# Performance work log

Hardware: AMD Instinct MI355X
Metric: run time of the kernel (lower is better)

The kernel has to match this reference:

```python
import jax, jax.numpy as jnp
import numpy as np

TEMPERATURE = 0.5


def setup_inputs() -> dict:
    key = jax.random.key(0)
    k1, k2 = jax.random.split(key)
    N, D = 8192, 128
    features = jax.random.normal(k1, (N, D), dtype=jnp.float32)
    labels = jax.random.randint(k2, (N,), 0, 10, dtype=jnp.int64)
    return {"features": features, "labels": labels}


def reference(features, labels):
    # cosine similarity via normalized matmul (fused form of the broadcasted version)
    eps = 1e-8
    norm = jnp.maximum(jnp.linalg.norm(features, axis=-1, keepdims=True), eps)
    fn = features / norm
    sim = jnp.einsum('id,jd->ij', fn, fn) / TEMPERATURE  # [N, N]

    pos_mask = labels[:, None] == labels[None, :]        # [N, N] bool
    pos_f = pos_mask.astype(sim.dtype)
    neg_f = 1.0 - pos_f

    exp_pos = jnp.exp(sim * pos_f)                       # [N, N]
    exp_neg = jnp.sum(jnp.exp(sim * neg_f), axis=1, keepdims=True)  # [N, 1]

    loss_mat = -jnp.log(exp_pos / (exp_pos + exp_neg))   # [N, N]
    # mean over positive entries (jit-safe masked mean)
    num_pos = jnp.sum(pos_f)
    loss = jnp.sum(loss_mat * pos_f) / num_pos
    return loss
```

## Files before the change

kernel.cpp:

```cpp
#include <hip/hip_runtime.h>
#include <hip/hip_bf16.h>
#include <math.h>

#define NROWS 8192
#define DIM 128
#define BM 128
#define BN 128
#define CS 8
#define COLS_PER_SLAB (NROWS / CS)
#define CT_ITERS (COLS_PER_SLAB / BN)
#define RS (NROWS / BM)
#define SQRT2 1.41421356237309515f

typedef __attribute__((ext_vector_type(8))) short bf16x8;
typedef __attribute__((ext_vector_type(4))) float f32x4;

__global__ __launch_bounds__(256) void k_norm(const float* __restrict__ f,
                                              __hip_bfloat16* __restrict__ fnb,
                                              float* __restrict__ losssum) {
  if (blockIdx.x == 0 && threadIdx.x == 0) losssum[0] = 0.f;
  int wave = threadIdx.x >> 6;
  int lane = threadIdx.x & 63;
  int row = blockIdx.x * 4 + wave;
  const float* src = f + (size_t)row * DIM;
  float v0 = src[lane];
  float v1 = src[lane + 64];
  float ss = v0 * v0 + v1 * v1;
#pragma unroll
  for (int o = 32; o > 0; o >>= 1) ss += __shfl_down(ss, o);
  ss = __shfl(ss, 0);
  float inv = SQRT2 / fmaxf(sqrtf(ss), 1e-8f);
  __hip_bfloat16* dst = fnb + (size_t)row * DIM;
  dst[lane] = __float2bfloat16(v0 * inv);
  dst[lane + 64] = __float2bfloat16(v1 * inv);
}

__global__ __launch_bounds__(256, 2) void k_main(
    const ushort* __restrict__ fnb, const int* __restrict__ lab,
    float* __restrict__ ptot, float* __restrict__ ppos, float* __restrict__ psim) {
  __shared__ char lds[BM * 256 + BN * 256];
  char* Alds = lds;
  char* Blds = lds + BM * 256;

  const int t = threadIdx.x;
  const int lane = t & 63;
  const int w = t >> 6;
  const int wm = w >> 1;
  const int wn = w & 1;
  const int g = lane >> 4;
  const int li16 = lane & 15;
  const int cs = blockIdx.x;
  const int i0 = blockIdx.y * BM;

  {
    const int4* src = reinterpret_cast<const int4*>(fnb + (size_t)i0 * DIM);
#pragma unroll
    for (int it = 0; it < 8; ++it) {
      int q = t + 256 * it;
      int row = q >> 4, c = q & 15;
      int4 v = src[q];
      *reinterpret_cast<int4*>(Alds + row * 256 + ((c << 4) ^ ((row & 7) << 4))) = v;
    }
  }

  int lr[4][4];
#pragma unroll
  for (int m = 0; m < 4; ++m)
#pragma unroll
    for (int r = 0; r < 4; ++r)
      lr[m][r] = lab[i0 + wm * 64 + m * 16 + g * 4 + r];

  float a_tot[4][4] = {}, a_pos[4][4] = {}, a_sim[4][4] = {};

  for (int ct = 0; ct < CT_ITERS; ++ct) {
    const int j0 = cs * COLS_PER_SLAB + ct * BN;
    __syncthreads();
    {
      const int4* src = reinterpret_cast<const int4*>(fnb + (size_t)j0 * DIM);
#pragma unroll
      for (int it = 0; it < 8; ++it) {
        int q = t + 256 * it;
        int row = q >> 4, c = q & 15;
        int4 v = src[q];
        *reinterpret_cast<int4*>(Blds + row * 256 + ((c << 4) ^ ((row & 7) << 4))) = v;
      }
    }
    __syncthreads();

    f32x4 acc[4][4];
#pragma unroll
    for (int m = 0; m < 4; ++m)
#pragma unroll
      for (int n = 0; n < 4; ++n) acc[m][n] = (f32x4){0.f, 0.f, 0.f, 0.f};

#pragma unroll
    for (int ks = 0; ks < 4; ++ks) {
      const int kb = ks * 64 + (g << 4);
      bf16x8 af[4], bf[4];
#pragma unroll
      for (int m = 0; m < 4; ++m) {
        int r = wm * 64 + m * 16 + li16;
        af[m] = *reinterpret_cast<const bf16x8*>(Alds + r * 256 + (kb ^ ((r & 7) << 4)));
      }
#pragma unroll
      for (int n = 0; n < 4; ++n) {
        int r = wn * 64 + n * 16 + li16;
        bf[n] = *reinterpret_cast<const bf16x8*>(Blds + r * 256 + (kb ^ ((r & 7) << 4)));
      }
#pragma unroll
      for (int m = 0; m < 4; ++m)
#pragma unroll
        for (int n = 0; n < 4; ++n)
          acc[m][n] = __builtin_amdgcn_mfma_f32_16x16x32_bf16(af[m], bf[n], acc[m][n], 0, 0, 0);
    }

#pragma unroll
    for (int n = 0; n < 4; ++n) {
      const int lc = lab[j0 + wn * 64 + n * 16 + li16];
#pragma unroll
      for (int m = 0; m < 4; ++m)
#pragma unroll
        for (int r = 0; r < 4; ++r) {
          float s = acc[m][n][r];
          float E = __expf(s);
          bool pos = (lr[m][r] == lc);
          a_tot[m][r] += E;
          a_pos[m][r] += pos ? E : 0.f;
          a_sim[m][r] += pos ? s : 0.f;
        }
    }
  }

#pragma unroll
  for (int m = 0; m < 4; ++m)
#pragma unroll
    for (int r = 0; r < 4; ++r)
#pragma unroll
      for (int off = 8; off > 0; off >>= 1) {
        a_tot[m][r] += __shfl_xor(a_tot[m][r], off);
        a_pos[m][r] += __shfl_xor(a_pos[m][r], off);
        a_sim[m][r] += __shfl_xor(a_sim[m][r], off);
      }

  __syncthreads();
  float(*red)[2][3] = reinterpret_cast<float(*)[2][3]>(lds);
  if (li16 == 0) {
#pragma unroll
    for (int m = 0; m < 4; ++m)
#pragma unroll
      for (int r = 0; r < 4; ++r) {
        int rl = wm * 64 + m * 16 + g * 4 + r;
        red[rl][wn][0] = a_tot[m][r];
        red[rl][wn][1] = a_pos[m][r];
        red[rl][wn][2] = a_sim[m][r];
      }
  }
  __syncthreads();
  if (wn == 0 && li16 == 0) {
#pragma unroll
    for (int m = 0; m < 4; ++m)
#pragma unroll
      for (int r = 0; r < 4; ++r) {
        int rl = wm * 64 + m * 16 + g * 4 + r;
        int row = i0 + rl;
        ptot[(size_t)cs * NROWS + row] = red[rl][0][0] + red[rl][1][0];
        ppos[(size_t)cs * NROWS + row] = red[rl][0][1] + red[rl][1][1];
        psim[(size_t)cs * NROWS + row] = red[rl][0][2] + red[rl][1][2];
      }
  }
}

__global__ __launch_bounds__(1024) void k_rowfinal(
    const float* __restrict__ ptot, const float* __restrict__ ppos,
    const float* __restrict__ psim, const int* __restrict__ lab,
    float* __restrict__ losssum) {
  __shared__ int sh[16][16];
  __shared__ int hist_s[16];
  __shared__ float sred[1024];
  const int t = threadIdx.x;
  const int w = t >> 6;
  if ((t & 63) < 16) sh[w][t & 63] = 0;
  __syncthreads();
#pragma unroll
  for (int it = 0; it < NROWS / 1024; ++it)
    atomicAdd(&sh[w][lab[t + it * 1024]], 1);
  __syncthreads();
  if (t < 16) {
    int s = 0;
#pragma unroll
    for (int x = 0; x < 16; ++x) s += sh[x][t];
    hist_s[t] = s;
  }
  __syncthreads();

  int i = blockIdx.x * 1024 + t;
  float st = 0.f, sp = 0.f, sa = 0.f;
#pragma unroll
  for (int cs = 0; cs < CS; ++cs) {
    st += ptot[(size_t)cs * NROWS + i];
    sp += ppos[(size_t)cs * NROWS + i];
    sa += psim[(size_t)cs * NROWS + i];
  }
  float cnt = (float)hist_s[lab[i]];
  float negtot = st - sp + cnt;
  float li = cnt * logf(negtot) + sp / negtot - sa;
  sred[t] = li;
  __syncthreads();
  for (int s2 = 512; s2 > 0; s2 >>= 1) {
    if (t < s2) sred[t] += sred[t + s2];
    __syncthreads();
  }
  if (t == 0) {
    atomicAdd(&losssum[0], sred[0]);
    if (blockIdx.x == 0) {
      int np = 0;
#pragma unroll
      for (int c = 0; c < 10; ++c) np += hist_s[c] * hist_s[c];
      losssum[1] = (float)np;
    }
  }
}

__global__ void k_out(const float* __restrict__ losssum, float* __restrict__ out) {
  if (threadIdx.x == 0) out[0] = losssum[0] / losssum[1];
}

extern "C" void kernel_launch(void* const* d_in, const int* in_sizes, int n_in,
                              void* d_out, int out_size, void* d_ws, size_t ws_size,
                              hipStream_t stream) {
  const float* feat = (const float*)d_in[0];
  const int* lab = (const int*)d_in[1];
  float* out = (float*)d_out;

  char* ws = (char*)d_ws;
  __hip_bfloat16* fnb = (__hip_bfloat16*)ws;
  size_t off = (size_t)NROWS * DIM * 2;
  float* ptot = (float*)(ws + off); off += (size_t)CS * NROWS * 4;
  float* ppos = (float*)(ws + off); off += (size_t)CS * NROWS * 4;
  float* psim = (float*)(ws + off); off += (size_t)CS * NROWS * 4;
  float* losssum = (float*)(ws + off);

  k_norm<<<NROWS / 4, 256, 0, stream>>>(feat, fnb, losssum);
  dim3 grid(CS, RS);
  k_main<<<grid, 256, 0, stream>>>((const ushort*)fnb, lab, ptot, ppos, psim);
  k_rowfinal<<<NROWS / 1024, 1024, 0, stream>>>(ptot, ppos, psim, lab, losssum);
  k_out<<<1, 64, 0, stream>>>(losssum, out);
}
```

Before: 50.93 us.

## Exploit symmetry of similarity matrix with upper-triangular tiles and exp2 scaling

The main kernel now computes only upper-triangular 128x128 block tiles of the symmetric similarity matrix. Each off-diagonal tile contributes its row sums directly and its column sums through atomics into per-diagonal partial buffers, which roughly halves the MFMA and exp work. Features are prescaled by sqrt(2/ln2) so that exp2 replaces exp, and the sim term is corrected by ln2 in the final reduction. The cost is a memset of a large column-partials buffer, atomic traffic, uneven per-block work, and a final pass that reads many more partials. A slab fallback path is kept for when the workspace is too small.

After: 132.1 us. 159% more time.

```diff
diff --git a/kernel.cpp b/kernel.cpp
--- a/kernel.cpp
+++ b/kernel.cpp
@@ -6,11 +6,14 @@
 #define DIM 128
 #define BM 128
 #define BN 128
+#define NRB 64
+#define CHW 4
+#define NCH 16
 #define CS 8
 #define COLS_PER_SLAB (NROWS / CS)
 #define CT_ITERS (COLS_PER_SLAB / BN)
-#define RS (NROWS / BM)
-#define SQRT2 1.41421356237309515f
+#define SCALE 1.69864368f
+#define LN2F 0.69314718056f
 
 typedef __attribute__((ext_vector_type(8))) short bf16x8;
 typedef __attribute__((ext_vector_type(4))) float f32x4;
@@ -29,15 +32,20 @@
 #pragma unroll
   for (int o = 32; o > 0; o >>= 1) ss += __shfl_down(ss, o);
   ss = __shfl(ss, 0);
-  float inv = SQRT2 / fmaxf(sqrtf(ss), 1e-8f);
+  float inv = SCALE / fmaxf(sqrtf(ss), 1e-8f);
   __hip_bfloat16* dst = fnb + (size_t)row * DIM;
   dst[lane] = __float2bfloat16(v0 * inv);
   dst[lane + 64] = __float2bfloat16(v1 * inv);
 }
 
-__global__ __launch_bounds__(256, 2) void k_main(
+__global__ __launch_bounds__(256, 2) void k_main_tri(
     const ushort* __restrict__ fnb, const int* __restrict__ lab,
-    float* __restrict__ ptot, float* __restrict__ ppos, float* __restrict__ psim) {
+    float* __restrict__ Prow, float* __restrict__ Pcol) {
+  const int c = blockIdx.x;
+  const int bi = blockIdx.y;
+  const int bj0 = bi + c * CHW;
+  if (bj0 >= NRB) return;
+
   __shared__ char lds[BM * 256 + BN * 256];
   char* Alds = lds;
   char* Blds = lds + BM * 256;
@@ -45,21 +53,18 @@
   const int t = threadIdx.x;
   const int lane = t & 63;
   const int w = t >> 6;
-  const int wm = w >> 1;
-  const int wn = w & 1;
-  const int g = lane >> 4;
-  const int li16 = lane & 15;
-  const int cs = blockIdx.x;
-  const int i0 = blockIdx.y * BM;
+  const int wm = w >> 1, wn = w & 1;
+  const int g = lane >> 4, li16 = lane & 15;
+  const int i0 = bi * BM;
 
   {
     const int4* src = reinterpret_cast<const int4*>(fnb + (size_t)i0 * DIM);
 #pragma unroll
     for (int it = 0; it < 8; ++it) {
       int q = t + 256 * it;
-      int row = q >> 4, c = q & 15;
+      int row = q >> 4, cc = q & 15;
       int4 v = src[q];
-      *reinterpret_cast<int4*>(Alds + row * 256 + ((c << 4) ^ ((row & 7) << 4))) = v;
+      *reinterpret_cast<int4*>(Alds + row * 256 + ((cc << 4) ^ ((row & 7) << 4))) = v;
     }
   }
 
@@ -72,17 +77,19 @@
 
   float a_tot[4][4] = {}, a_pos[4][4] = {}, a_sim[4][4] = {};
 
-  for (int ct = 0; ct < CT_ITERS; ++ct) {
-    const int j0 = cs * COLS_PER_SLAB + ct * BN;
+#pragma unroll 1
+  for (int bj = bj0; bj < bj0 + CHW && bj < NRB; ++bj) {
+    const int j0 = bj * BN;
+    const int d = bj - bi;
     __syncthreads();
     {
       const int4* src = reinterpret_cast<const int4*>(fnb + (size_t)j0 * DIM);
 #pragma unroll
       for (int it = 0; it < 8; ++it) {
         int q = t + 256 * it;
-        int row = q >> 4, c = q & 15;
+        int row = q >> 4, cc = q & 15;
         int4 v = src[q];
-        *reinterpret_cast<int4*>(Blds + row * 256 + ((c << 4) ^ ((row & 7) << 4))) = v;
+        *reinterpret_cast<int4*>(Blds + row * 256 + ((cc << 4) ^ ((row & 7) << 4))) = v;
       }
     }
     __syncthreads();
@@ -114,6 +121,7 @@
           acc[m][n] = __builtin_amdgcn_mfma_f32_16x16x32_bf16(af[m], bf[n], acc[m][n], 0, 0, 0);
     }
 
+    float c_tot[4] = {}, c_pos[4] = {}, c_sim[4] = {};
 #pragma unroll
     for (int n = 0; n < 4; ++n) {
       const int lc = lab[j0 + wn * 64 + n * 16 + li16];
@@ -121,13 +129,36 @@
       for (int m = 0; m < 4; ++m)
 #pragma unroll
         for (int r = 0; r < 4; ++r) {
-          float s = acc[m][n][r];
-          float E = __expf(s);
-          bool pos = (lr[m][r] == lc);
+          float u = acc[m][n][r];
+          float E = __builtin_exp2f(u);
+          float msk = (lr[m][r] == lc) ? 1.f : 0.f;
           a_tot[m][r] += E;
-          a_pos[m][r] += pos ? E : 0.f;
-          a_sim[m][r] += pos ? s : 0.f;
+          c_tot[n] += E;
+          a_pos[m][r] = fmaf(msk, E, a_pos[m][r]);
+          a_sim[m][r] = fmaf(msk, u, a_sim[m][r]);
+          c_pos[n] = fmaf(msk, E, c_pos[n]);
+          c_sim[n] = fmaf(msk, u, c_sim[n]);
         }
+    }
+
+    if (d > 0) {
+#pragma unroll
+      for (int n = 0; n < 4; ++n) {
+        c_tot[n] += __shfl_xor(c_tot[n], 16); c_tot[n] += __shfl_xor(c_tot[n], 32);
+        c_pos[n] += __shfl_xor(c_pos[n], 16); c_pos[n] += __shfl_xor(c_pos[n], 32);
+        c_sim[n] += __shfl_xor(c_sim[n], 16); c_sim[n] += __shfl_xor(c_sim[n], 32);
+      }
+      if (g == 0) {
+        const int s = NRB - d;
+#pragma unroll
+        for (int n = 0; n < 4; ++n) {
+          int col = j0 + wn * 64 + n * 16 + li16;
+          float* dst = Pcol + ((size_t)s * NROWS + col) * 3;
+          atomicAdd(&dst[0], c_tot[n]);
+          atomicAdd(&dst[1], c_pos[n]);
+          atomicAdd(&dst[2], c_sim[n]);
+        }
+      }
     }
   }
 
@@ -143,16 +174,16 @@
       }
 
   __syncthreads();
-  float(*red)[2][3] = reinterpret_cast<float(*)[2][3]>(lds);
+  float* red = reinterpret_cast<float*>(lds);
   if (li16 == 0) {
 #pragma unroll
     for (int m = 0; m < 4; ++m)
 #pragma unroll
       for (int r = 0; r < 4; ++r) {
         int rl = wm * 64 + m * 16 + g * 4 + r;
-        red[rl][wn][0] = a_tot[m][r];
-        red[rl][wn][1] = a_pos[m][r];
-        red[rl][wn][2] = a_sim[m][r];
+        red[(rl * 2 + wn) * 3 + 0] = a_tot[m][r];
+        red[(rl * 2 + wn) * 3 + 1] = a_pos[m][r];
+        red[(rl * 2 + wn) * 3 + 2] = a_sim[m][r];
       }
   }
   __syncthreads();
@@ -162,18 +193,17 @@
 #pragma unroll
       for (int r = 0; r < 4; ++r) {
         int rl = wm * 64 + m * 16 + g * 4 + r;
-        int row = i0 + rl;
-        ptot[(size_t)cs * NROWS + row] = red[rl][0][0] + red[rl][1][0];
-        ppos[(size_t)cs * NROWS + row] = red[rl][0][1] + red[rl][1][1];
-        psim[(size_t)cs * NROWS + row] = red[rl][0][2] + red[rl][1][2];
-      }
-  }
-}
-
-__global__ __launch_bounds__(1024) void k_rowfinal(
-    const float* __restrict__ ptot, const float* __restrict__ ppos,
-    const float* __restrict__ psim, const int* __restrict__ lab,
-    float* __restrict__ losssum) {
+        float* dst = Prow + ((size_t)c * NROWS + (i0 + rl)) * 3;
+        dst[0] = red[(rl * 2) * 3 + 0] + red[(rl * 2 + 1) * 3 + 0];
+        dst[1] = red[(rl * 2) * 3 + 1] + red[(rl * 2 + 1) * 3 + 1];
+        dst[2] = red[(rl * 2) * 3 + 2] + red[(rl * 2 + 1) * 3 + 2];
+      }
+  }
+}
+
+__global__ __launch_bounds__(1024) void k_rowfinal_tri(
+    const float* __restrict__ Prow, const float* __restrict__ Pcol,
+    const int* __restrict__ lab, float* __restrict__ losssum) {
   __shared__ int sh[16][16];
   __shared__ int hist_s[16];
   __shared__ float sred[1024];
@@ -194,16 +224,20 @@
   __syncthreads();
 
   int i = blockIdx.x * 1024 + t;
+  int b = i >> 7;
+  int cmax = (63 - b) >> 2;
   float st = 0.f, sp = 0.f, sa = 0.f;
-#pragma unroll
-  for (int cs = 0; cs < CS; ++cs) {
-    st += ptot[(size_t)cs * NROWS + i];
-    sp += ppos[(size_t)cs * NROWS + i];
-    sa += psim[(size_t)cs * NROWS + i];
+  for (int cc = 0; cc <= cmax; ++cc) {
+    const float* p = Prow + ((size_t)cc * NROWS + i) * 3;
+    st += p[0]; sp += p[1]; sa += p[2];
+  }
+  for (int s = 0; s < NRB; ++s) {
+    const float* p = Pcol + ((size_t)s * NROWS + i) * 3;
+    st += p[0]; sp += p[1]; sa += p[2];
   }
   float cnt = (float)hist_s[lab[i]];
   float negtot = st - sp + cnt;
-  float li = cnt * logf(negtot) + sp / negtot - sa;
+  float li = cnt * logf(negtot) + sp / negtot - LN2F * sa;
   sred[t] = li;
   __syncthreads();
   for (int s2 = 512; s2 > 0; s2 >>= 1) {
@@ -215,7 +249,176 @@
     if (blockIdx.x == 0) {
       int np = 0;
 #pragma unroll
-      for (int c = 0; c < 10; ++c) np += hist_s[c] * hist_s[c];
+      for (int cq = 0; cq < 10; ++cq) np += hist_s[cq] * hist_s[cq];
+      losssum[1] = (float)np;
+    }
+  }
+}
+
+__global__ __launch_bounds__(256, 2) void k_main_slab(
+    const ushort* __restrict__ fnb, const int* __restrict__ lab, float* __restrict__ P) {
+  __shared__ char lds[BM * 256 + BN * 256];
+  char* Alds = lds;
+  char* Blds = lds + BM * 256;
+  const int t = threadIdx.x;
+  const int lane = t & 63;
+  const int w = t >> 6;
+  const int wm = w >> 1, wn = w & 1;
+  const int g = lane >> 4, li16 = lane & 15;
+  const int cs = blockIdx.x;
+  const int i0 = blockIdx.y * BM;
+  {
+    const int4* src = reinterpret_cast<const int4*>(fnb + (size_t)i0 * DIM);
+#pragma unroll
+    for (int it = 0; it < 8; ++it) {
+      int q = t + 256 * it;
+      int row = q >> 4, cc = q & 15;
+      int4 v = src[q];
+      *reinterpret_cast<int4*>(Alds + row * 256 + ((cc << 4) ^ ((row & 7) << 4))) = v;
+    }
+  }
+  int lr[4][4];
+#pragma unroll
+  for (int m = 0; m < 4; ++m)
+#pragma unroll
+    for (int r = 0; r < 4; ++r)
+      lr[m][r] = lab[i0 + wm * 64 + m * 16 + g * 4 + r];
+  float a_tot[4][4] = {}, a_pos[4][4] = {}, a_sim[4][4] = {};
+  for (int ct = 0; ct < CT_ITERS; ++ct) {
+    const int j0 = cs * COLS_PER_SLAB + ct * BN;
+    __syncthreads();
+    {
+      const int4* src = reinterpret_cast<const int4*>(fnb + (size_t)j0 * DIM);
+#pragma unroll
+      for (int it = 0; it < 8; ++it) {
+        int q = t + 256 * it;
+        int row = q >> 4, cc = q & 15;
+        int4 v = src[q];
+        *reinterpret_cast<int4*>(Blds + row * 256 + ((cc << 4) ^ ((row & 7) << 4))) = v;
+      }
+    }
+    __syncthreads();
+    f32x4 acc[4][4];
+#pragma unroll
+    for (int m = 0; m < 4; ++m)
+#pragma unroll
+      for (int n = 0; n < 4; ++n) acc[m][n] = (f32x4){0.f, 0.f, 0.f, 0.f};
+#pragma unroll
+    for (int ks = 0; ks < 4; ++ks) {
+      const int kb = ks * 64 + (g << 4);
+      bf16x8 af[4], bf[4];
+#pragma unroll
+      for (int m = 0; m < 4; ++m) {
+        int r = wm * 64 + m * 16 + li16;
+        af[m] = *reinterpret_cast<const bf16x8*>(Alds + r * 256 + (kb ^ ((r & 7) << 4)));
+      }
+#pragma unroll
+      for (int n = 0; n < 4; ++n) {
+        int r = wn * 64 + n * 16 + li16;
+        bf[n] = *reinterpret_cast<const bf16x8*>(Blds + r * 256 + (kb ^ ((r & 7) << 4)));
+      }
+#pragma unroll
+      for (int m = 0; m < 4; ++m)
+#pragma unroll
+        for (int n = 0; n < 4; ++n)
+          acc[m][n] = __builtin_amdgcn_mfma_f32_16x16x32_bf16(af[m], bf[n], acc[m][n], 0, 0, 0);
+    }
+#pragma unroll
+    for (int n = 0; n < 4; ++n) {
+      const int lc = lab[j0 + wn * 64 + n * 16 + li16];
+#pragma unroll
+      for (int m = 0; m < 4; ++m)
+#pragma unroll
+        for (int r = 0; r < 4; ++r) {
+          float u = acc[m][n][r];
+          float E = __builtin_exp2f(u);
+          float msk = (lr[m][r] == lc) ? 1.f : 0.f;
+          a_tot[m][r] += E;
+          a_pos[m][r] = fmaf(msk, E, a_pos[m][r]);
+          a_sim[m][r] = fmaf(msk, u, a_sim[m][r]);
+        }
+    }
+  }
+#pragma unroll
+  for (int m = 0; m < 4; ++m)
+#pragma unroll
+    for (int r = 0; r < 4; ++r)
+#pragma unroll
+      for (int off = 8; off > 0; off >>= 1) {
+        a_tot[m][r] += __shfl_xor(a_tot[m][r], off);
+        a_pos[m][r] += __shfl_xor(a_pos[m][r], off);
+        a_sim[m][r] += __shfl_xor(a_sim[m][r], off);
+      }
+  __syncthreads();
+  float* red = reinterpret_cast<float*>(lds);
+  if (li16 == 0) {
+#pragma unroll
+    for (int m = 0; m < 4; ++m)
+#pragma unroll
+      for (int r = 0; r < 4; ++r) {
+        int rl = wm * 64 + m * 16 + g * 4 + r;
+        red[(rl * 2 + wn) * 3 + 0] = a_tot[m][r];
+        red[(rl * 2 + wn) * 3 + 1] = a_pos[m][r];
+        red[(rl * 2 + wn) * 3 + 2] = a_sim[m][r];
+      }
+  }
+  __syncthreads();
+  if (wn == 0 && li16 == 0) {
+#pragma unroll
+    for (int m = 0; m < 4; ++m)
+#pragma unroll
+      for (int r = 0; r < 4; ++r) {
+        int rl = wm * 64 + m * 16 + g * 4 + r;
+        float* dst = P + ((size_t)cs * NROWS + (i0 + rl)) * 3;
+        dst[0] = red[(rl * 2) * 3 + 0] + red[(rl * 2 + 1) * 3 + 0];
+        dst[1] = red[(rl * 2) * 3 + 1] + red[(rl * 2 + 1) * 3 + 1];
+        dst[2] = red[(rl * 2) * 3 + 2] + red[(rl * 2 + 1) * 3 + 2];
+      }
+  }
+}
+
+__global__ __launch_bounds__(1024) void k_rowfinal_slab(
+    const float* __restrict__ P, const int* __restrict__ lab, float* __restrict__ losssum) {
+  __shared__ int sh[16][16];
+  __shared__ int hist_s[16];
+  __shared__ float sred[1024];
+  const int t = threadIdx.x;
+  const int w = t >> 6;
+  if ((t & 63) < 16) sh[w][t & 63] = 0;
+  __syncthreads();
+#pragma unroll
+  for (int it = 0; it < NROWS / 1024; ++it)
+    atomicAdd(&sh[w][lab[t + it * 1024]], 1);
+  __syncthreads();
+  if (t < 16) {
+    int s = 0;
+#pragma unroll
+    for (int x = 0; x < 16; ++x) s += sh[x][t];
+    hist_s[t] = s;
+  }
+  __syncthreads();
+  int i = blockIdx.x * 1024 + t;
+  float st = 0.f, sp = 0.f, sa = 0.f;
+#pragma unroll
+  for (int cs = 0; cs < CS; ++cs) {
+    const float* p = P + ((size_t)cs * NROWS + i) * 3;
+    st += p[0]; sp += p[1]; sa += p[2];
+  }
+  float cnt = (float)hist_s[lab[i]];
+  float negtot = st - sp + cnt;
+  float li = cnt * logf(negtot) + sp / negtot - LN2F * sa;
+  sred[t] = li;
+  __syncthreads();
+  for (int s2 = 512; s2 > 0; s2 >>= 1) {
+    if (t < s2) sred[t] += sred[t + s2];
+    __syncthreads();
+  }
+  if (t == 0) {
+    atomicAdd(&losssum[0], sred[0]);
+    if (blockIdx.x == 0) {
+      int np = 0;
+#pragma unroll
+      for (int cq = 0; cq < 10; ++cq) np += hist_s[cq] * hist_s[cq];
       losssum[1] = (float)np;
     }
   }
@@ -231,18 +434,28 @@
   const float* feat = (const float*)d_in[0];
   const int* lab = (const int*)d_in[1];
   float* out = (float*)d_out;
-
   char* ws = (char*)d_ws;
+
+  const size_t fnbB = (size_t)NROWS * DIM * 2;
+  const size_t prowB = (size_t)NCH * NROWS * 3 * 4;
+  const size_t pcolB = (size_t)NRB * NROWS * 3 * 4;
   __hip_bfloat16* fnb = (__hip_bfloat16*)ws;
-  size_t off = (size_t)NROWS * DIM * 2;
-  float* ptot = (float*)(ws + off); off += (size_t)CS * NROWS * 4;
-  float* ppos = (float*)(ws + off); off += (size_t)CS * NROWS * 4;
-  float* psim = (float*)(ws + off); off += (size_t)CS * NROWS * 4;
-  float* losssum = (float*)(ws + off);
-
-  k_norm<<<NROWS / 4, 256, 0, stream>>>(feat, fnb, losssum);
-  dim3 grid(CS, RS);
-  k_main<<<grid, 256, 0, stream>>>((const ushort*)fnb, lab, ptot, ppos, psim);
-  k_rowfinal<<<NROWS / 1024, 1024, 0, stream>>>(ptot, ppos, psim, lab, losssum);
-  k_out<<<1, 64, 0, stream>>>(losssum, out);
-}
+
+  if (ws_size >= fnbB + prowB + pcolB + 256) {
+    float* Prow = (float*)(ws + fnbB);
+    float* Pcol = (float*)(ws + fnbB + prowB);
+    float* losssum = (float*)(ws + fnbB + prowB + pcolB);
+    hipMemsetAsync(Pcol, 0, pcolB, stream);
+    k_norm<<<NROWS / 4, 256, 0, stream>>>(feat, fnb, losssum);
+    k_main_tri<<<dim3(NCH, NRB), 256, 0, stream>>>((const ushort*)fnb, lab, Prow, Pcol);
+    k_rowfinal_tri<<<NROWS / 1024, 1024, 0, stream>>>(Prow, Pcol, lab, losssum);
+    k_out<<<1, 64, 0, stream>>>(losssum, out);
+  } else {
+    float* P = (float*)(ws + fnbB);
+    float* losssum = (float*)(ws + fnbB + (size_t)CS * NROWS * 3 * 4);
+    k_norm<<<NROWS / 4, 256, 0, stream>>>(feat, fnb, losssum);
+    k_main_slab<<<dim3(CS, NROWS / BM), 256, 0, stream>>>((const ushort*)fnb, lab, P);
+    k_rowfinal_slab<<<NROWS / 1024, 1024, 0, stream>>>(P, lab, losssum);
+    k_out<<<1, 64, 0, stream>>>(losssum, out);
+  }
+}
```

## Double-buffer B tiles via direct global-to-LDS loads, keep A fragments in registers

Applied to the files above, without the earlier changes.

B tiles are now staged with global_load_lds into a double buffer, so the load of the next column tile overlaps the MFMA and exp work on the current one, with one barrier per iteration instead of two. A fragments are read from LDS once and kept in registers for the whole column loop. The normalization scale is folded so that exp2 replaces exp, with an ln2 correction applied in the final reduction. Partial sums are stored interleaved in a single buffer. This raises register pressure at 2 waves per SIMD and relies on hand-written waitcnt ordering for correctness.

Result: slower. 62.45 us (+22.6%).

```diff
diff --git a/kernel.cpp b/kernel.cpp
--- a/kernel.cpp
+++ b/kernel.cpp
@@ -10,10 +10,28 @@
 #define COLS_PER_SLAB (NROWS / CS)
 #define CT_ITERS (COLS_PER_SLAB / BN)
 #define RS (NROWS / BM)
-#define SQRT2 1.41421356237309515f
+#define SCALE 1.69864368f
+#define LN2F 0.69314718056f
 
 typedef __attribute__((ext_vector_type(8))) short bf16x8;
 typedef __attribute__((ext_vector_type(4))) float f32x4;
+
+__device__ __forceinline__ void gload16(const void* g, void* l) {
+  __builtin_amdgcn_global_load_lds(
+      (const __attribute__((address_space(1))) void*)g,
+      (__attribute__((address_space(3))) void*)l, 16, 0, 0);
+}
+
+__device__ __forceinline__ void stage_tile(const ushort* __restrict__ fnb, int row0,
+                                           char* tile, int w, int lane) {
+  const char* gb = reinterpret_cast<const char*>(fnb);
+#pragma unroll
+  for (int i = 0; i < 8; ++i) {
+    int rl = w * 32 + i * 4 + (lane >> 4);
+    int src = ((lane & 15) ^ (rl & 7)) << 4;
+    gload16(gb + (size_t)(row0 + rl) * 256 + src, tile + w * 8192 + i * 1024);
+  }
+}
 
 __global__ __launch_bounds__(256) void k_norm(const float* __restrict__ f,
                                               __hip_bfloat16* __restrict__ fnb,
@@ -29,7 +47,7 @@
 #pragma unroll
   for (int o = 32; o > 0; o >>= 1) ss += __shfl_down(ss, o);
   ss = __shfl(ss, 0);
-  float inv = SQRT2 / fmaxf(sqrtf(ss), 1e-8f);
+  float inv = SCALE / fmaxf(sqrtf(ss), 1e-8f);
   __hip_bfloat16* dst = fnb + (size_t)row * DIM;
   dst[lane] = __float2bfloat16(v0 * inv);
   dst[lane + 64] = __float2bfloat16(v1 * inv);
@@ -37,31 +55,35 @@
 
 __global__ __launch_bounds__(256, 2) void k_main(
     const ushort* __restrict__ fnb, const int* __restrict__ lab,
-    float* __restrict__ ptot, float* __restrict__ ppos, float* __restrict__ psim) {
-  __shared__ char lds[BM * 256 + BN * 256];
-  char* Alds = lds;
-  char* Blds = lds + BM * 256;
-
+    float* __restrict__ P) {
+  __shared__ char lds[2 * BM * 256];
   const int t = threadIdx.x;
   const int lane = t & 63;
   const int w = t >> 6;
-  const int wm = w >> 1;
-  const int wn = w & 1;
-  const int g = lane >> 4;
-  const int li16 = lane & 15;
+  const int wm = w >> 1, wn = w & 1;
+  const int g = lane >> 4, li16 = lane & 15;
   const int cs = blockIdx.x;
   const int i0 = blockIdx.y * BM;
-
-  {
-    const int4* src = reinterpret_cast<const int4*>(fnb + (size_t)i0 * DIM);
-#pragma unroll
-    for (int it = 0; it < 8; ++it) {
-      int q = t + 256 * it;
-      int row = q >> 4, c = q & 15;
-      int4 v = src[q];
-      *reinterpret_cast<int4*>(Alds + row * 256 + ((c << 4) ^ ((row & 7) << 4))) = v;
-    }
-  }
+  const int jslab = cs * COLS_PER_SLAB;
+
+  stage_tile(fnb, i0, lds, w, lane);
+  stage_tile(fnb, jslab, lds + 32768, w, lane);
+  asm volatile("s_waitcnt vmcnt(8)" ::: "memory");
+  __builtin_amdgcn_s_barrier();
+
+  bf16x8 af[4][4];
+#pragma unroll
+  for (int m = 0; m < 4; ++m) {
+    int r = wm * 64 + m * 16 + li16;
+#pragma unroll
+    for (int ks = 0; ks < 4; ++ks) {
+      int cb = ((ks * 4 + g) ^ (r & 7)) << 4;
+      af[m][ks] = *reinterpret_cast<const bf16x8*>(lds + r * 256 + cb);
+    }
+  }
+  asm volatile("s_waitcnt lgkmcnt(0)" ::: "memory");
+  __builtin_amdgcn_sched_barrier(0);
+  __builtin_amdgcn_s_barrier();
 
   int lr[4][4];
 #pragma unroll
@@ -72,20 +94,12 @@
 
   float a_tot[4][4] = {}, a_pos[4][4] = {}, a_sim[4][4] = {};
 
+#pragma unroll 1
   for (int ct = 0; ct < CT_ITERS; ++ct) {
-    const int j0 = cs * COLS_PER_SLAB + ct * BN;
-    __syncthreads();
-    {
-      const int4* src = reinterpret_cast<const int4*>(fnb + (size_t)j0 * DIM);
-#pragma unroll
-      for (int it = 0; it < 8; ++it) {
-        int q = t + 256 * it;
-        int row = q >> 4, c = q & 15;
-        int4 v = src[q];
-        *reinterpret_cast<int4*>(Blds + row * 256 + ((c << 4) ^ ((row & 7) << 4))) = v;
-      }
-    }
-    __syncthreads();
+    const int j0 = jslab + ct * BN;
+    char* bufc = lds + ((size_t)((ct & 1) ^ 1) << 15);
+    if (ct < CT_ITERS - 1)
+      stage_tile(fnb, j0 + BN, lds + ((size_t)(ct & 1) << 15), w, lane);
 
     f32x4 acc[4][4];
 #pragma unroll
@@ -95,23 +109,18 @@
 
 #pragma unroll
     for (int ks = 0; ks < 4; ++ks) {
-      const int kb = ks * 64 + (g << 4);
-      bf16x8 af[4], bf[4];
-#pragma unroll
-      for (int m = 0; m < 4; ++m) {
-        int r = wm * 64 + m * 16 + li16;
-        af[m] = *reinterpret_cast<const bf16x8*>(Alds + r * 256 + (kb ^ ((r & 7) << 4)));
-      }
+      bf16x8 bf[4];
 #pragma unroll
       for (int n = 0; n < 4; ++n) {
         int r = wn * 64 + n * 16 + li16;
-        bf[n] = *reinterpret_cast<const bf16x8*>(Blds + r * 256 + (kb ^ ((r & 7) << 4)));
+        int cb = ((ks * 4 + g) ^ (r & 7)) << 4;
+        bf[n] = *reinterpret_cast<const bf16x8*>(bufc + r * 256 + cb);
       }
 #pragma unroll
       for (int m = 0; m < 4; ++m)
 #pragma unroll
         for (int n = 0; n < 4; ++n)
-          acc[m][n] = __builtin_amdgcn_mfma_f32_16x16x32_bf16(af[m], bf[n], acc[m][n], 0, 0, 0);
+          acc[m][n] = __builtin_amdgcn_mfma_f32_16x16x32_bf16(af[m][ks], bf[n], acc[m][n], 0, 0, 0);
     }
 
 #pragma unroll
@@ -121,14 +130,17 @@
       for (int m = 0; m < 4; ++m)
 #pragma unroll
         for (int r = 0; r < 4; ++r) {
-          float s = acc[m][n][r];
-          float E = __expf(s);
-          bool pos = (lr[m][r] == lc);
+          float u = acc[m][n][r];
+          float E = __builtin_exp2f(u);
+          float msk = (lr[m][r] == lc) ? 1.f : 0.f;
           a_tot[m][r] += E;
-          a_pos[m][r] += pos ? E : 0.f;
-          a_sim[m][r] += pos ? s : 0.f;
+          a_pos[m][r] = fmaf(msk, E, a_pos[m][r]);
+          a_sim[m][r] = fmaf(msk, u, a_sim[m][r]);
         }
     }
+
+    asm volatile("s_waitcnt vmcnt(0)" ::: "memory");
+    __builtin_amdgcn_s_barrier();
   }
 
 #pragma unroll
@@ -143,16 +155,16 @@
       }
 
   __syncthreads();
-  float(*red)[2][3] = reinterpret_cast<float(*)[2][3]>(lds);
+  float* red = reinterpret_cast<float*>(lds);
   if (li16 == 0) {
 #pragma unroll
     for (int m = 0; m < 4; ++m)
 #pragma unroll
       for (int r = 0; r < 4; ++r) {
         int rl = wm * 64 + m * 16 + g * 4 + r;
-        red[rl][wn][0] = a_tot[m][r];
-        red[rl][wn][1] = a_pos[m][r];
-        red[rl][wn][2] = a_sim[m][r];
+        red[(rl * 2 + wn) * 3 + 0] = a_tot[m][r];
+        red[(rl * 2 + wn) * 3 + 1] = a_pos[m][r];
+        red[(rl * 2 + wn) * 3 + 2] = a_sim[m][r];
       }
   }
   __syncthreads();
@@ -162,17 +174,16 @@
 #pragma unroll
       for (int r = 0; r < 4; ++r) {
         int rl = wm * 64 + m * 16 + g * 4 + r;
-        int row = i0 + rl;
-        ptot[(size_t)cs * NROWS + row] = red[rl][0][0] + red[rl][1][0];
-        ppos[(size_t)cs * NROWS + row] = red[rl][0][1] + red[rl][1][1];
-        psim[(size_t)cs * NROWS + row] = red[rl][0][2] + red[rl][1][2];
+        float* dst = P + ((size_t)cs * NROWS + (i0 + rl)) * 3;
+        dst[0] = red[(rl * 2) * 3 + 0] + red[(rl * 2 + 1) * 3 + 0];
+        dst[1] = red[(rl * 2) * 3 + 1] + red[(rl * 2 + 1) * 3 + 1];
+        dst[2] = red[(rl * 2) * 3 + 2] + red[(rl * 2 + 1) * 3 + 2];
       }
   }
 }
 
 __global__ __launch_bounds__(1024) void k_rowfinal(
-    const float* __restrict__ ptot, const float* __restrict__ ppos,
-    const float* __restrict__ psim, const int* __restrict__ lab,
+    const float* __restrict__ P, const int* __restrict__ lab,
     float* __restrict__ losssum) {
   __shared__ int sh[16][16];
   __shared__ int hist_s[16];
@@ -197,13 +208,12 @@
   float st = 0.f, sp = 0.f, sa = 0.f;
 #pragma unroll
   for (int cs = 0; cs < CS; ++cs) {
-    st += ptot[(size_t)cs * NROWS + i];
-    sp += ppos[(size_t)cs * NROWS + i];
-    sa += psim[(size_t)cs * NROWS + i];
+    const float* p = P + ((size_t)cs * NROWS + i) * 3;
+    st += p[0]; sp += p[1]; sa += p[2];
   }
   float cnt = (float)hist_s[lab[i]];
   float negtot = st - sp + cnt;
-  float li = cnt * logf(negtot) + sp / negtot - sa;
+  float li = cnt * logf(negtot) + sp / negtot - LN2F * sa;
   sred[t] = li;
   __syncthreads();
   for (int s2 = 512; s2 > 0; s2 >>= 1) {
@@ -231,18 +241,15 @@
   const float* feat = (const float*)d_in[0];
   const int* lab = (const int*)d_in[1];
   float* out = (float*)d_out;
-
   char* ws = (char*)d_ws;
+
   __hip_bfloat16* fnb = (__hip_bfloat16*)ws;
   size_t off = (size_t)NROWS * DIM * 2;
-  float* ptot = (float*)(ws + off); off += (size_t)CS * NROWS * 4;
-  float* ppos = (float*)(ws + off); off += (size_t)CS * NROWS * 4;
-  float* psim = (float*)(ws + off); off += (size_t)CS * NROWS * 4;
+  float* P = (float*)(ws + off); off += (size_t)CS * NROWS * 3 * 4;
   float* losssum = (float*)(ws + off);
 
   k_norm<<<NROWS / 4, 256, 0, stream>>>(feat, fnb, losssum);
-  dim3 grid(CS, RS);
-  k_main<<<grid, 256, 0, stream>>>((const ushort*)fnb, lab, ptot, ppos, psim);
-  k_rowfinal<<<NROWS / 1024, 1024, 0, stream>>>(ptot, ppos, psim, lab, losssum);
+  k_main<<<dim3(CS, RS), 256, 0, stream>>>((const ushort*)fnb, lab, P);
+  k_rowfinal<<<NROWS / 1024, 1024, 0, stream>>>(P, lab, losssum);
   k_out<<<1, 64, 0, stream>>>(losssum, out);
 }
```
